# Kernel tuning notes

Hardware: AMD Instinct MI355X
Metric: run time of the kernel (lower is better)

Reference implementation:

```python
import jax, jax.numpy as jnp
import numpy as np

N_PDE = 4096
SENSOR_RANGE = 0.08
WINDOW = int(SENSOR_RANGE * N_PDE)   # 327
HALF = WINDOW // 2                   # 163
RESIZE_LEN = 20
FREQS = jnp.array([1.0, 2.0, 4.0, 8.0], dtype=jnp.float32)
EPS = 1e-6  # flax GroupNorm default epsilon
U_MAX, V_MAX = 40.0, 1.0
N_AGENTS = 262144


def setup_inputs() -> dict:
    key = jax.random.key(0)
    ks = jax.random.split(key, 16)

    def w(k, shape):
        fan_in = shape[0]
        return (jax.random.normal(k, shape, jnp.float32) / np.float32(np.sqrt(fan_in)))

    return {
        "z_curr": jax.random.normal(ks[0], (N_PDE,), jnp.float32),
        "z_target": jax.random.normal(ks[1], (N_PDE,), jnp.float32),
        "xi_curr": jax.random.uniform(ks[2], (N_AGENTS,), jnp.float32),
        # branch net (features=[256,256]), each layer: Dense + GroupNorm(1 group) + tanh
        "bW0": w(ks[3], (2 * RESIZE_LEN, 256)), "bb0": jnp.zeros((256,), jnp.float32),
        "bs0": jnp.ones((256,), jnp.float32), "bB0": jnp.zeros((256,), jnp.float32),
        "bW1": w(ks[4], (256, 256)), "bb1": jnp.zeros((256,), jnp.float32),
        "bs1": jnp.ones((256,), jnp.float32), "bB1": jnp.zeros((256,), jnp.float32),
        # trunk net: 8 -> 32 -> 32
        "tW0": w(ks[5], (8, 32)), "tb0": jnp.zeros((32,), jnp.float32),
        "tW1": w(ks[6], (32, 32)), "tb1": jnp.zeros((32,), jnp.float32),
        # combined head: (256+32) -> 32, then two 32 -> 1 heads
        "cW": w(ks[7], (256 + 32, 32)), "cb": jnp.zeros((32,), jnp.float32),
        "uW": w(ks[8], (32, 1)), "ub": jnp.zeros((1,), jnp.float32),
        "vW": w(ks[9], (32, 1)), "vb": jnp.zeros((1,), jnp.float32),
    }


def _local_obs(padded_error, xi):
    # per-agent dynamic slice + finite-difference gradient + bilinear resize
    center = (xi * (N_PDE - 1)).astype(jnp.int32) + HALF
    start = center - HALF
    p_err = jax.lax.dynamic_slice(padded_error, (start,), (WINDOW,))
    p_grad = jnp.gradient(p_err)
    p_err = jax.image.resize(p_err, (RESIZE_LEN,), method='bilinear')
    p_grad = jax.image.resize(p_grad, (RESIZE_LEN,), method='bilinear')
    return jnp.concatenate([p_err, p_grad])  # [40]


def _groupnorm1(x, scale, bias):
    # GroupNorm(num_groups=1) applied per-sample over the feature axis
    mu = jnp.mean(x, axis=-1, keepdims=True)
    var = jnp.var(x, axis=-1, keepdims=True)
    return (x - mu) * jax.lax.rsqrt(var + EPS) * scale + bias


def reference(z_curr, z_target, xi_curr,
              bW0, bb0, bs0, bB0, bW1, bb1, bs1, bB1,
              tW0, tb0, tW1, tb1, cW, cb, uW, ub, vW, vb):
    error = z_curr - z_target
    padded = jnp.pad(error, (HALF, HALF), mode='edge')  # [N_PDE + 2*HALF]

    patches = jax.vmap(lambda xi: _local_obs(padded, xi))(xi_curr)  # [A, 40]

    # branch net
    h = jnp.tanh(_groupnorm1(patches @ bW0 + bb0, bs0, bB0))  # [A, 256]
    h = jnp.tanh(_groupnorm1(h @ bW1 + bb1, bs1, bB1))        # [A, 256]

    # trunk net
    angle = xi_curr[:, None] * FREQS * jnp.pi                 # [A, 4]
    enc = jnp.concatenate([jnp.sin(angle), jnp.cos(angle)], axis=-1)  # [A, 8]
    enc = jnp.tanh(enc @ tW0 + tb0)
    enc = jnp.tanh(enc @ tW1 + tb1)                           # [A, 32]

    combined = jnp.concatenate([h, enc], axis=-1)             # [A, 288]
    x = jnp.tanh(combined @ cW + cb)                          # [A, 32]
    u_raw = (x @ uW + ub).squeeze(-1)
    v_raw = (x @ vW + vb).squeeze(-1)
    return (U_MAX * jnp.tanh(u_raw), V_MAX * jnp.tanh(v_raw))
```

## Files before the change

kernel.cpp:

```cpp
#include <hip/hip_runtime.h>

#define NP      4096
#define WINDOW  327
#define HALF    163
#define RL      20
#define NA      262144
#define GN_EPS  1e-6f
#define R       4
#define NBLK    (NP / R)

__device__ __forceinline__ float tanh_fast(float x) {
  float e = __expf(2.0f * x);
  return 1.0f - 2.0f / (e + 1.0f);
}

__device__ __forceinline__ void wave_sum2(float& a, float& b) {
#pragma unroll
  for (int m = 1; m < 64; m <<= 1) {
    a += __shfl_xor(a, m, 64);
    b += __shfl_xor(b, m, 64);
  }
}

#define L_ESP   0
#define L_OBS   332
#define L_HBUF  492
#define L_PART  1532
#define L_HCL   5628
#define L_TOT   5772

__global__ __launch_bounds__(256, 4) void dc_table(
    const float* __restrict__ zc,  const float* __restrict__ zt,
    const float* __restrict__ bW0, const float* __restrict__ bb0,
    const float* __restrict__ bs0, const float* __restrict__ bB0,
    const float* __restrict__ bW1, const float* __restrict__ bb1,
    const float* __restrict__ bs1, const float* __restrict__ bB1,
    const float* __restrict__ tW0, const float* __restrict__ tb0,
    const float* __restrict__ tW1, const float* __restrict__ tb1,
    const float* __restrict__ cW,  const float* __restrict__ cb,
    const float* __restrict__ uW,  const float* __restrict__ ub,
    const float* __restrict__ vW,  const float* __restrict__ vb,
    float* __restrict__ tbl)
{
  __shared__ __align__(16) float sm[L_TOT];
  float* espan = sm + L_ESP;
  float* obsT  = sm + L_OBS;
  float* hbuf  = sm + L_HBUF;
  float* part  = sm + L_PART;
  float* hcL   = sm + L_HCL;

  const int tid = threadIdx.x;
  const int w   = tid >> 6;
  const int l   = tid & 63;
  const int s0  = blockIdx.x * R;

  for (int t = tid; t < WINDOW + R - 1; t += 256) {
    int c = s0 - HALF + t;
    c = c < 0 ? 0 : (c > NP - 1 ? NP - 1 : c);
    espan[t] = zc[c] - zt[c];
  }
  __syncthreads();

  {
    const float INV  = (float)WINDOW / (float)RL;
    const float RINV = (float)RL / (float)WINDOW;
    int task = tid;
    if (task < R * 2 * RL) {
      int q = task % (2 * RL);
      int r = task / (2 * RL);
      int qq = (q < RL) ? q : q - RL;
      float xs = ((float)qq + 0.5f) * INV - 0.5f;
      int jlo = (int)ceilf(xs - INV);  if (jlo < 0) jlo = 0;
      int jhi = (int)floorf(xs + INV); if (jhi > WINDOW - 1) jhi = WINDOW - 1;
      const float* p = espan + r;
      float wsum = 0.0f, acc = 0.0f;
      for (int j = jlo; j <= jhi; ++j) {
        float wq = 1.0f - fabsf(xs - (float)j) * RINV;
        float v;
        if (q < RL) {
          v = p[j];
        } else {
          v = (j == 0) ? (p[1] - p[0]) :
              (j == WINDOW - 1) ? (p[WINDOW - 1] - p[WINDOW - 2]) :
              0.5f * (p[j + 1] - p[j - 1]);
        }
        wsum += wq;
        acc  += wq * v;
      }
      obsT[q * 4 + r] = acc / wsum;
    }
  }
  __syncthreads();

  float acc[R][4];

#pragma unroll
  for (int r = 0; r < R; ++r) { acc[r][0]=0.f; acc[r][1]=0.f; acc[r][2]=0.f; acc[r][3]=0.f; }
#pragma unroll 2
  for (int kk = 0; kk < 10; ++kk) {
    int k = w * 10 + kk;
    float4 wt = *(const float4*)&bW0[k * 256 + 4 * l];
    float4 o  = *(const float4*)&obsT[k * 4];
    const float wv[4] = {wt.x, wt.y, wt.z, wt.w};
    const float ov[4] = {o.x, o.y, o.z, o.w};
#pragma unroll
    for (int r = 0; r < R; ++r)
#pragma unroll
      for (int j = 0; j < 4; ++j) acc[r][j] = fmaf(ov[r], wv[j], acc[r][j]);
  }

  {
#pragma unroll
    for (int r = 0; r < R; ++r)
      *(float4*)&part[w * 1024 + r * 256 + 4 * l] = make_float4(acc[r][0], acc[r][1], acc[r][2], acc[r][3]);
    __syncthreads();
    int rr = w, g = l;
    float val[4];
    {
      float4 b0 = *(const float4*)&bb0[4 * g];
      val[0]=b0.x; val[1]=b0.y; val[2]=b0.z; val[3]=b0.w;
    }
#pragma unroll
    for (int w2 = 0; w2 < 4; ++w2) {
      float4 p0 = *(const float4*)&part[w2 * 1024 + rr * 256 + 4 * g];
      val[0]+=p0.x; val[1]+=p0.y; val[2]+=p0.z; val[3]+=p0.w;
    }
    float s = 0.f, q = 0.f;
#pragma unroll
    for (int i = 0; i < 4; ++i) { s += val[i]; q += val[i] * val[i]; }
    wave_sum2(s, q);
    float mu  = s * (1.0f / 256.0f);
    float var = fmaxf(q * (1.0f / 256.0f) - mu * mu, 0.0f);
    float rv  = rsqrtf(var + GN_EPS);
    float4 sc0 = *(const float4*)&bs0[4 * g];
    float4 sh0 = *(const float4*)&bB0[4 * g];
    const float sc[4] = {sc0.x,sc0.y,sc0.z,sc0.w};
    const float sh[4] = {sh0.x,sh0.y,sh0.z,sh0.w};
    float h[4];
#pragma unroll
    for (int i = 0; i < 4; ++i) h[i] = tanh_fast((val[i] - mu) * rv * sc[i] + sh[i]);
    *(float4*)&hbuf[rr * 260 + 4 * g] = make_float4(h[0], h[1], h[2], h[3]);
  }
  __syncthreads();

#pragma unroll
  for (int r = 0; r < R; ++r) { acc[r][0]=0.f; acc[r][1]=0.f; acc[r][2]=0.f; acc[r][3]=0.f; }
#pragma unroll 2
  for (int kk = 0; kk < 64; kk += 4) {
    int k0 = w * 64 + kk;
    float4 wt0 = *(const float4*)&bW1[(k0    ) * 256 + 4 * l];
    float4 wt1 = *(const float4*)&bW1[(k0 + 1) * 256 + 4 * l];
    float4 wt2 = *(const float4*)&bW1[(k0 + 2) * 256 + 4 * l];
    float4 wt3 = *(const float4*)&bW1[(k0 + 3) * 256 + 4 * l];
    float4 hr[R];
#pragma unroll
    for (int r = 0; r < R; ++r) hr[r] = *(const float4*)&hbuf[r * 260 + k0];
#pragma unroll
    for (int r = 0; r < R; ++r) {
      const float* hp = (const float*)&hr[r];
      acc[r][0] = fmaf(hp[0], wt0.x, acc[r][0]); acc[r][1] = fmaf(hp[0], wt0.y, acc[r][1]);
      acc[r][2] = fmaf(hp[0], wt0.z, acc[r][2]); acc[r][3] = fmaf(hp[0], wt0.w, acc[r][3]);
      acc[r][0] = fmaf(hp[1], wt1.x, acc[r][0]); acc[r][1] = fmaf(hp[1], wt1.y, acc[r][1]);
      acc[r][2] = fmaf(hp[1], wt1.z, acc[r][2]); acc[r][3] = fmaf(hp[1], wt1.w, acc[r][3]);
      acc[r][0] = fmaf(hp[2], wt2.x, acc[r][0]); acc[r][1] = fmaf(hp[2], wt2.y, acc[r][1]);
      acc[r][2] = fmaf(hp[2], wt2.z, acc[r][2]); acc[r][3] = fmaf(hp[2], wt2.w, acc[r][3]);
      acc[r][0] = fmaf(hp[3], wt3.x, acc[r][0]); acc[r][1] = fmaf(hp[3], wt3.y, acc[r][1]);
      acc[r][2] = fmaf(hp[3], wt3.z, acc[r][2]); acc[r][3] = fmaf(hp[3], wt3.w, acc[r][3]);
    }
  }

  {
#pragma unroll
    for (int r = 0; r < R; ++r)
      *(float4*)&part[w * 1024 + r * 256 + 4 * l] = make_float4(acc[r][0], acc[r][1], acc[r][2], acc[r][3]);
    __syncthreads();
    int rr = w, g = l;
    float val[4];
    {
      float4 b0 = *(const float4*)&bb1[4 * g];
      val[0]=b0.x; val[1]=b0.y; val[2]=b0.z; val[3]=b0.w;
    }
#pragma unroll
    for (int w2 = 0; w2 < 4; ++w2) {
      float4 p0 = *(const float4*)&part[w2 * 1024 + rr * 256 + 4 * g];
      val[0]+=p0.x; val[1]+=p0.y; val[2]+=p0.z; val[3]+=p0.w;
    }
    float s = 0.f, q = 0.f;
#pragma unroll
    for (int i = 0; i < 4; ++i) { s += val[i]; q += val[i] * val[i]; }
    wave_sum2(s, q);
    float mu  = s * (1.0f / 256.0f);
    float var = fmaxf(q * (1.0f / 256.0f) - mu * mu, 0.0f);
    float rv  = rsqrtf(var + GN_EPS);
    float4 sc0 = *(const float4*)&bs1[4 * g];
    float4 sh0 = *(const float4*)&bB1[4 * g];
    const float sc[4] = {sc0.x,sc0.y,sc0.z,sc0.w};
    const float sh[4] = {sh0.x,sh0.y,sh0.z,sh0.w};
    float h[4];
#pragma unroll
    for (int i = 0; i < 4; ++i) h[i] = tanh_fast((val[i] - mu) * rv * sc[i] + sh[i]);
    *(float4*)&hbuf[rr * 260 + 4 * g] = make_float4(h[0], h[1], h[2], h[3]);
  }
  __syncthreads();

  {
    int r = w;
    int c = l & 31;
    int kh = (l >> 5) * 128;
    float ga = (l < 32) ? cb[c] : 0.0f;
#pragma unroll 4
    for (int k = kh; k < kh + 128; k += 4) {
      float4 hv = *(const float4*)&hbuf[r * 260 + k];
      ga = fmaf(hv.x, cW[(k    ) * 32 + c], ga);
      ga = fmaf(hv.y, cW[(k + 1) * 32 + c], ga);
      ga = fmaf(hv.z, cW[(k + 2) * 32 + c], ga);
      ga = fmaf(hv.w, cW[(k + 3) * 32 + c], ga);
    }
    ga += __shfl_xor(ga, 32, 64);
    if (l < 32) hcL[r * 36 + c] = ga;
  }
  __syncthreads();

  if (tid < 64) {
    int v = tid >> 3, sub = tid & 7;
    int r = v >> 1, e = v & 1;
    int jg = s0 + r + e;
    float xe = (float)jg * (1.0f / 4095.0f);
    float enc[8];
#pragma unroll
    for (int k = 0; k < 4; ++k) {
      float fr = (float)(1 << k);
      float a = (xe * fr) * 3.14159265358979f;
      enc[k]     = sinf(a);
      enc[k + 4] = cosf(a);
    }
    int base = tid & ~7;

    float t0v[4];
#pragma unroll
    for (int i = 0; i < 4; ++i) {
      int f = 4 * sub + i;
      float a = tb0[f];
#pragma unroll
      for (int k = 0; k < 8; ++k) a = fmaf(enc[k], tW0[k * 32 + f], a);
      t0v[i] = tanh_fast(a);
    }

    float t1v[4];
#pragma unroll
    for (int i = 0; i < 4; ++i) t1v[i] = tb1[4 * sub + i];
#pragma unroll
    for (int j8 = 0; j8 < 8; ++j8) {
#pragma unroll
      for (int i2 = 0; i2 < 4; ++i2) {
        float tv = __shfl(t0v[i2], base + j8, 64);
        int k = 4 * j8 + i2;
#pragma unroll
        for (int i = 0; i < 4; ++i) t1v[i] = fmaf(tv, tW1[k * 32 + 4 * sub + i], t1v[i]);
      }
    }
#pragma unroll
    for (int i = 0; i < 4; ++i) t1v[i] = tanh_fast(t1v[i]);

    float xvv[4];
#pragma unroll
    for (int i = 0; i < 4; ++i) xvv[i] = hcL[r * 36 + 4 * sub + i];
#pragma unroll
    for (int j8 = 0; j8 < 8; ++j8) {
#pragma unroll
      for (int i2 = 0; i2 < 4; ++i2) {
        float tv = __shfl(t1v[i2], base + j8, 64);
        int k = 4 * j8 + i2;
#pragma unroll
        for (int i = 0; i < 4; ++i) xvv[i] = fmaf(tv, cW[(256 + k) * 32 + 4 * sub + i], xvv[i]);
      }
    }
#pragma unroll
    for (int i = 0; i < 4; ++i) xvv[i] = tanh_fast(xvv[i]);

    float up = 0.f, vp = 0.f;
#pragma unroll
    for (int i = 0; i < 4; ++i) {
      up = fmaf(xvv[i], uW[4 * sub + i], up);
      vp = fmaf(xvv[i], vW[4 * sub + i], vp);
    }
#pragma unroll
    for (int m = 1; m < 8; m <<= 1) {
      up += __shfl_xor(up, m, 64);
      vp += __shfl_xor(vp, m, 64);
    }
    if (sub == 0) {
      int s = s0 + r;
      tbl[4 * s + e]     = 40.0f * tanh_fast(up + ub[0]);
      tbl[4 * s + 2 + e] = tanh_fast(vp + vb[0]);
    }
  }
}

__global__ __launch_bounds__(256) void dc_agents(
    const float* __restrict__ xi_curr, const float4* __restrict__ tbl,
    float* __restrict__ out)
{
  int a = blockIdx.x * 256 + threadIdx.x;
  float xi = xi_curr[a];
  float p = xi * 4095.0f;
  int s = (int)p;
  s = s > 4095 ? 4095 : s;
  float t = p - (float)s;
  float4 tb = tbl[s];
  out[a]      = fmaf(t, tb.y - tb.x, tb.x);
  out[NA + a] = fmaf(t, tb.w - tb.z, tb.z);
}

extern "C" void kernel_launch(void* const* d_in, const int* in_sizes, int n_in,
                              void* d_out, int out_size, void* d_ws, size_t ws_size,
                              hipStream_t stream) {
  const float* zc  = (const float*)d_in[0];
  const float* zt  = (const float*)d_in[1];
  const float* xi  = (const float*)d_in[2];
  const float* bW0 = (const float*)d_in[3];
  const float* bb0 = (const float*)d_in[4];
  const float* bs0 = (const float*)d_in[5];
  const float* bB0 = (const float*)d_in[6];
  const float* bW1 = (const float*)d_in[7];
  const float* bb1 = (const float*)d_in[8];
  const float* bs1 = (const float*)d_in[9];
  const float* bB1 = (const float*)d_in[10];
  const float* tW0 = (const float*)d_in[11];
  const float* tb0 = (const float*)d_in[12];
  const float* tW1 = (const float*)d_in[13];
  const float* tb1 = (const float*)d_in[14];
  const float* cW  = (const float*)d_in[15];
  const float* cb  = (const float*)d_in[16];
  const float* uW  = (const float*)d_in[17];
  const float* ub  = (const float*)d_in[18];
  const float* vW  = (const float*)d_in[19];
  const float* vb  = (const float*)d_in[20];

  float* tbl = (float*)d_ws;
  float* out = (float*)d_out;

  dc_table<<<NBLK, 256, 0, stream>>>(zc, zt, bW0, bb0, bs0, bB0,
                                     bW1, bb1, bs1, bB1,
                                     tW0, tb0, tW1, tb1, cW, cb,
                                     uW, ub, vW, vb, tbl);
  dc_agents<<<NA / 256, 256, 0, stream>>>(xi, (const float4*)tbl, out);
}
```

Measured before the change: 123.4 us.

## Double table-kernel block to 512 threads, split K across 8 waves, vectorize head matvec

```diff
diff --git a/kernel.cpp b/kernel.cpp
--- a/kernel.cpp
+++ b/kernel.cpp
@@ -8,6 +8,7 @@
 #define GN_EPS  1e-6f
 #define R       4
 #define NBLK    (NP / R)
+#define NT      512
 
 __device__ __forceinline__ float tanh_fast(float x) {
   float e = __expf(2.0f * x);
@@ -24,12 +25,12 @@
 
 #define L_ESP   0
 #define L_OBS   332
-#define L_HBUF  492
-#define L_PART  1532
-#define L_HCL   5628
-#define L_TOT   5772
-
-__global__ __launch_bounds__(256, 4) void dc_table(
+#define L_PART  0
+#define L_HBUF  8192
+#define L_HCL   9232
+#define L_TOT   9376
+
+__global__ __launch_bounds__(NT, 8) void dc_table(
     const float* __restrict__ zc,  const float* __restrict__ zt,
     const float* __restrict__ bW0, const float* __restrict__ bb0,
     const float* __restrict__ bs0, const float* __restrict__ bB0,
@@ -45,8 +46,8 @@
   __shared__ __align__(16) float sm[L_TOT];
   float* espan = sm + L_ESP;
   float* obsT  = sm + L_OBS;
+  float* part  = sm + L_PART;
   float* hbuf  = sm + L_HBUF;
-  float* part  = sm + L_PART;
   float* hcL   = sm + L_HCL;
 
   const int tid = threadIdx.x;
@@ -54,41 +55,38 @@
   const int l   = tid & 63;
   const int s0  = blockIdx.x * R;
 
-  for (int t = tid; t < WINDOW + R - 1; t += 256) {
-    int c = s0 - HALF + t;
+  if (tid < WINDOW + R - 1) {
+    int c = s0 - HALF + tid;
     c = c < 0 ? 0 : (c > NP - 1 ? NP - 1 : c);
-    espan[t] = zc[c] - zt[c];
-  }
-  __syncthreads();
-
-  {
+    espan[tid] = zc[c] - zt[c];
+  }
+  __syncthreads();
+
+  if (tid < R * 2 * RL) {
     const float INV  = (float)WINDOW / (float)RL;
     const float RINV = (float)RL / (float)WINDOW;
-    int task = tid;
-    if (task < R * 2 * RL) {
-      int q = task % (2 * RL);
-      int r = task / (2 * RL);
-      int qq = (q < RL) ? q : q - RL;
-      float xs = ((float)qq + 0.5f) * INV - 0.5f;
-      int jlo = (int)ceilf(xs - INV);  if (jlo < 0) jlo = 0;
-      int jhi = (int)floorf(xs + INV); if (jhi > WINDOW - 1) jhi = WINDOW - 1;
-      const float* p = espan + r;
-      float wsum = 0.0f, acc = 0.0f;
-      for (int j = jlo; j <= jhi; ++j) {
-        float wq = 1.0f - fabsf(xs - (float)j) * RINV;
-        float v;
-        if (q < RL) {
-          v = p[j];
-        } else {
-          v = (j == 0) ? (p[1] - p[0]) :
-              (j == WINDOW - 1) ? (p[WINDOW - 1] - p[WINDOW - 2]) :
-              0.5f * (p[j + 1] - p[j - 1]);
-        }
-        wsum += wq;
-        acc  += wq * v;
+    int q = tid % (2 * RL);
+    int r = tid / (2 * RL);
+    int qq = (q < RL) ? q : q - RL;
+    float xs = ((float)qq + 0.5f) * INV - 0.5f;
+    int jlo = (int)ceilf(xs - INV);  if (jlo < 0) jlo = 0;
+    int jhi = (int)floorf(xs + INV); if (jhi > WINDOW - 1) jhi = WINDOW - 1;
+    const float* p = espan + r;
+    float wsum = 0.0f, acc = 0.0f;
+    for (int j = jlo; j <= jhi; ++j) {
+      float wq = 1.0f - fabsf(xs - (float)j) * RINV;
+      float v;
+      if (q < RL) {
+        v = p[j];
+      } else {
+        v = (j == 0) ? (p[1] - p[0]) :
+            (j == WINDOW - 1) ? (p[WINDOW - 1] - p[WINDOW - 2]) :
+            0.5f * (p[j + 1] - p[j - 1]);
       }
-      obsT[q * 4 + r] = acc / wsum;
-    }
+      wsum += wq;
+      acc  += wq * v;
+    }
+    obsT[q * 4 + r] = acc / wsum;
   }
   __syncthreads();
 
@@ -96,9 +94,8 @@
 
 #pragma unroll
   for (int r = 0; r < R; ++r) { acc[r][0]=0.f; acc[r][1]=0.f; acc[r][2]=0.f; acc[r][3]=0.f; }
-#pragma unroll 2
-  for (int kk = 0; kk < 10; ++kk) {
-    int k = w * 10 + kk;
+  for (int kk = 0; kk < 5; ++kk) {
+    int k = w * 5 + kk;
     float4 wt = *(const float4*)&bW0[k * 256 + 4 * l];
     float4 o  = *(const float4*)&obsT[k * 4];
     const float wv[4] = {wt.x, wt.y, wt.z, wt.w};
@@ -108,20 +105,18 @@
 #pragma unroll
       for (int j = 0; j < 4; ++j) acc[r][j] = fmaf(ov[r], wv[j], acc[r][j]);
   }
-
-  {
-#pragma unroll
-    for (int r = 0; r < R; ++r)
-      *(float4*)&part[w * 1024 + r * 256 + 4 * l] = make_float4(acc[r][0], acc[r][1], acc[r][2], acc[r][3]);
-    __syncthreads();
+  __syncthreads();
+
+#pragma unroll
+  for (int r = 0; r < R; ++r)
+    *(float4*)&part[w * 1024 + r * 256 + 4 * l] = make_float4(acc[r][0], acc[r][1], acc[r][2], acc[r][3]);
+  __syncthreads();
+  if (w < 4) {
     int rr = w, g = l;
-    float val[4];
-    {
-      float4 b0 = *(const float4*)&bb0[4 * g];
-      val[0]=b0.x; val[1]=b0.y; val[2]=b0.z; val[3]=b0.w;
-    }
-#pragma unroll
-    for (int w2 = 0; w2 < 4; ++w2) {
+    float4 b0 = *(const float4*)&bb0[4 * g];
+    float val[4] = {b0.x, b0.y, b0.z, b0.w};
+#pragma unroll
+    for (int w2 = 0; w2 < 8; ++w2) {
       float4 p0 = *(const float4*)&part[w2 * 1024 + rr * 256 + 4 * g];
       val[0]+=p0.x; val[1]+=p0.y; val[2]+=p0.z; val[3]+=p0.w;
     }
@@ -145,9 +140,8 @@
 
 #pragma unroll
   for (int r = 0; r < R; ++r) { acc[r][0]=0.f; acc[r][1]=0.f; acc[r][2]=0.f; acc[r][3]=0.f; }
-#pragma unroll 2
-  for (int kk = 0; kk < 64; kk += 4) {
-    int k0 = w * 64 + kk;
+  for (int kk = 0; kk < 32; kk += 4) {
+    int k0 = w * 32 + kk;
     float4 wt0 = *(const float4*)&bW1[(k0    ) * 256 + 4 * l];
     float4 wt1 = *(const float4*)&bW1[(k0 + 1) * 256 + 4 * l];
     float4 wt2 = *(const float4*)&bW1[(k0 + 2) * 256 + 4 * l];
@@ -169,19 +163,16 @@
     }
   }
 
-  {
-#pragma unroll
-    for (int r = 0; r < R; ++r)
-      *(float4*)&part[w * 1024 + r * 256 + 4 * l] = make_float4(acc[r][0], acc[r][1], acc[r][2], acc[r][3]);
-    __syncthreads();
+#pragma unroll
+  for (int r = 0; r < R; ++r)
+    *(float4*)&part[w * 1024 + r * 256 + 4 * l] = make_float4(acc[r][0], acc[r][1], acc[r][2], acc[r][3]);
+  __syncthreads();
+  if (w < 4) {
     int rr = w, g = l;
-    float val[4];
-    {
-      float4 b0 = *(const float4*)&bb1[4 * g];
-      val[0]=b0.x; val[1]=b0.y; val[2]=b0.z; val[3]=b0.w;
-    }
-#pragma unroll
-    for (int w2 = 0; w2 < 4; ++w2) {
+    float4 b0 = *(const float4*)&bb1[4 * g];
+    float val[4] = {b0.x, b0.y, b0.z, b0.w};
+#pragma unroll
+    for (int w2 = 0; w2 < 8; ++w2) {
       float4 p0 = *(const float4*)&part[w2 * 1024 + rr * 256 + 4 * g];
       val[0]+=p0.x; val[1]+=p0.y; val[2]+=p0.z; val[3]+=p0.w;
     }
@@ -203,21 +194,37 @@
   }
   __syncthreads();
 
-  {
-    int r = w;
-    int c = l & 31;
-    int kh = (l >> 5) * 128;
-    float ga = (l < 32) ? cb[c] : 0.0f;
-#pragma unroll 4
-    for (int k = kh; k < kh + 128; k += 4) {
-      float4 hv = *(const float4*)&hbuf[r * 260 + k];
-      ga = fmaf(hv.x, cW[(k    ) * 32 + c], ga);
-      ga = fmaf(hv.y, cW[(k + 1) * 32 + c], ga);
-      ga = fmaf(hv.z, cW[(k + 2) * 32 + c], ga);
-      ga = fmaf(hv.w, cW[(k + 3) * 32 + c], ga);
-    }
-    ga += __shfl_xor(ga, 32, 64);
-    if (l < 32) hcL[r * 36 + c] = ga;
+  if (w < 4) {
+    int r  = w;
+    int kg = l >> 3;
+    int c  = (l & 7) * 4;
+    float ga0 = 0.f, ga1 = 0.f, ga2 = 0.f, ga3 = 0.f;
+#pragma unroll
+    for (int ii = 0; ii < 8; ++ii) {
+      int j  = (ii + kg) & 7;
+      int kb = kg * 32 + 4 * j;
+      float4 hv = *(const float4*)&hbuf[r * 260 + kb];
+      const float hvv[4] = {hv.x, hv.y, hv.z, hv.w};
+#pragma unroll
+      for (int i2 = 0; i2 < 4; ++i2) {
+        float4 cw = *(const float4*)&cW[(kb + i2) * 32 + c];
+        ga0 = fmaf(hvv[i2], cw.x, ga0);
+        ga1 = fmaf(hvv[i2], cw.y, ga1);
+        ga2 = fmaf(hvv[i2], cw.z, ga2);
+        ga3 = fmaf(hvv[i2], cw.w, ga3);
+      }
+    }
+#pragma unroll
+    for (int m = 8; m < 64; m <<= 1) {
+      ga0 += __shfl_xor(ga0, m, 64);
+      ga1 += __shfl_xor(ga1, m, 64);
+      ga2 += __shfl_xor(ga2, m, 64);
+      ga3 += __shfl_xor(ga3, m, 64);
+    }
+    if (l < 8) {
+      float4 cbv = *(const float4*)&cb[c];
+      *(float4*)&hcL[r * 36 + c] = make_float4(ga0 + cbv.x, ga1 + cbv.y, ga2 + cbv.z, ga3 + cbv.w);
+    }
   }
   __syncthreads();
 
@@ -340,9 +347,9 @@
   float* tbl = (float*)d_ws;
   float* out = (float*)d_out;
 
-  dc_table<<<NBLK, 256, 0, stream>>>(zc, zt, bW0, bb0, bs0, bB0,
-                                     bW1, bb1, bs1, bB1,
-                                     tW0, tb0, tW1, tb1, cW, cb,
-                                     uW, ub, vW, vb, tbl);
+  dc_table<<<NBLK, NT, 0, stream>>>(zc, zt, bW0, bb0, bs0, bB0,
+                                    bW1, bb1, bs1, bB1,
+                                    tW0, tb0, tW1, tb1, cW, cb,
+                                    uW, ub, vW, vb, tbl);
   dc_agents<<<NA / 256, 256, 0, stream>>>(xi, (const float4*)tbl, out);
 }
```

New measurement: 146.0 us. +18.3%, slower.
